# Optimization experiments

Hardware: AMD Instinct MI355X
Metric: run time of the kernel (lower is better)

Reference implementation:

```python
import jax, jax.numpy as jnp
import numpy as np

B, A, L, M, E = 4096, 64, 16, 4, 10
K = (4, 16, 32)
Q = (2, 4, 6)
P = (32, 128, 256)


def setup_inputs() -> dict:
    key = jax.random.key(0)
    ks = iter(jax.random.split(key, 32))
    inp = {}
    inp['x'] = jax.random.normal(next(ks), (B, A, L, M), dtype=jnp.float32)
    inp['y'] = jax.random.uniform(next(ks), (B, E), dtype=jnp.float32)
    inp['w1'] = jax.random.normal(next(ks), (E, K[0], Q[0], A), dtype=jnp.float32) / (K[0] * Q[0])
    inp['w2'] = jax.random.normal(next(ks), (E, K[1], Q[1], A), dtype=jnp.float32) / (K[1] * Q[1])
    inp['w3'] = jax.random.normal(next(ks), (E, K[2], Q[2], A), dtype=jnp.float32) / (K[2] * Q[2])
    inp['coeff1'] = jax.random.normal(next(ks), (P[0],), dtype=jnp.float32)
    inp['coeff2'] = jax.random.normal(next(ks), (P[1],), dtype=jnp.float32)
    inp['coeff3'] = jax.random.normal(next(ks), (P[2],), dtype=jnp.float32)
    ri = lambda n, hi: jax.random.randint(next(ks), (n,), 0, hi, dtype=jnp.int32)
    inp['i1'] = ri(P[0], L); inp['l1'] = ri(P[0], M)
    inp['k1'] = ri(P[0], K[0]); inp['q1'] = ri(P[0], Q[0])
    inp['i2'] = ri(P[1], L); inp['j2'] = ri(P[1], L)
    inp['l2'] = ri(P[1], M); inp['m2'] = ri(P[1], M)
    inp['k2'] = ri(P[1], K[1]); inp['q2'] = ri(P[1], Q[1])
    inp['i3'] = ri(P[2], L); inp['j3'] = ri(P[2], L); inp['f3'] = ri(P[2], L)
    inp['l3'] = ri(P[2], M); inp['m3'] = ri(P[2], M); inp['g3'] = ri(P[2], M)
    inp['k3'] = ri(P[2], K[2]); inp['q3'] = ri(P[2], Q[2])
    return inp


def _forward(x, y, w1, w2, w3, coeff1, coeff2, coeff3,
             i1, l1, k1, q1,
             i2, j2, l2, m2, k2, q2,
             i3, j3, f3, l3, m3, g3, k3, q3):
    # element-mixed weights: [B, K, Q, A]
    wy1 = jnp.einsum('ekqa,be->bkqa', w1, y)
    wy2 = jnp.einsum('ekqa,be->bkqa', w2, y)
    wy3 = jnp.einsum('ekqa,be->bkqa', w3, y)
    # sparse path contraction (equivalent to dense 'ik,lq,ekqa,bail,be->ba' etc.)
    g1 = jnp.transpose(wy1[:, k1, q1, :], (0, 2, 1))          # [B, A, P1]
    t1 = jnp.einsum('bap,p->ba', x[:, :, i1, l1] * g1, coeff1)
    g2 = jnp.transpose(wy2[:, k2, q2, :], (0, 2, 1))          # [B, A, P2]
    t2 = jnp.einsum('bap,p->ba', x[:, :, i2, l2] * x[:, :, j2, m2] * g2, coeff2)
    g3_ = jnp.transpose(wy3[:, k3, q3, :], (0, 2, 1))         # [B, A, P3]
    t3 = jnp.einsum('bap,p->ba',
                    x[:, :, i3, l3] * x[:, :, j3, m3] * x[:, :, f3, g3] * g3_,
                    coeff3)
    return t1 + t2 + t3  # [B, A] (scalar irrep_out -> flattened view)


def reference(x, y, w1, w2, w3, coeff1, coeff2, coeff3,
              i1, l1, k1, q1,
              i2, j2, l2, m2, k2, q2,
              i3, j3, f3, l3, m3, g3, k3, q3):
    return _forward(x, y, w1, w2, w3, coeff1, coeff2, coeff3,
                    i1, l1, k1, q1,
                    i2, j2, l2, m2, k2, q2,
                    i3, j3, f3, l3, m3, g3, k3, q3)
```

## Files before the change

### kernel.cpp

```cpp
#include <hip/hip_runtime.h>
#include <hip/hip_bf16.h>

typedef _Float16 f16x8 __attribute__((ext_vector_type(8)));
typedef _Float16 f16x4 __attribute__((ext_vector_type(4)));
typedef float    f32x4 __attribute__((ext_vector_type(4)));

constexpr int BB  = 4096;
constexpr int AA  = 64;
constexpr int ED  = 10;
constexpr int P1N = 32, P2N = 128, P3N = 256;
constexpr int PT  = 416;
constexpr int NKS = 13;
constexpr int BCH = 64;
constexpr int NCH = 4;

__global__ void build_idx_kernel(
    const int* __restrict__ i1, const int* __restrict__ l1,
    const int* __restrict__ i2, const int* __restrict__ j2,
    const int* __restrict__ l2, const int* __restrict__ m2,
    const int* __restrict__ i3, const int* __restrict__ j3,
    const int* __restrict__ f3, const int* __restrict__ l3,
    const int* __restrict__ m3, const int* __restrict__ g3,
    unsigned* __restrict__ idxs) {
  const int p = threadIdx.x;
  if (p >= PT) return;
  unsigned sa, sb = 64, sc = 64;
  if (p < P1N) {
    sa = i1[p] * 4 + l1[p];
  } else if (p < P1N + P2N) {
    int pp = p - P1N;
    sa = i2[pp] * 4 + l2[pp];
    sb = j2[pp] * 4 + m2[pp];
  } else {
    int pp = p - P1N - P2N;
    sa = i3[pp] * 4 + l3[pp];
    sb = j3[pp] * 4 + m3[pp];
    sc = f3[pp] * 4 + g3[pp];
  }
  idxs[p] = (sa * 8) | ((sb * 8) << 10) | ((sc * 8) << 20);
}

__global__ void build_cwb_kernel(
    const float* __restrict__ w1, const float* __restrict__ w2, const float* __restrict__ w3,
    const float* __restrict__ c1, const float* __restrict__ c2, const float* __restrict__ c3,
    const int* __restrict__ k1, const int* __restrict__ q1,
    const int* __restrict__ k2, const int* __restrict__ q2,
    const int* __restrict__ k3, const int* __restrict__ q3,
    _Float16* __restrict__ cwb) {
  const int a  = blockIdx.x & 63;
  const int ks = blockIdx.x >> 6;
  const int l  = threadIdx.x;
  const int grp = l >> 4, e = l & 15;
  _Float16* dst = cwb + (((size_t)a * NKS + ks) * 64 + l) * 8;
  #pragma unroll
  for (int j = 0; j < 8; ++j) {
    const int p = ks * 32 + grp * 8 + j;
    float v = 0.f;
    if (e < ED) {
      const float* w; float coeff; int k, q, K, Q;
      if (p < P1N)            { w = w1; coeff = c1[p]; k = k1[p]; q = q1[p]; K = 4;  Q = 2; }
      else if (p < P1N + P2N) { int pp = p - P1N;       w = w2; coeff = c2[pp]; k = k2[pp]; q = q2[pp]; K = 16; Q = 4; }
      else                    { int pp = p - P1N - P2N; w = w3; coeff = c3[pp]; k = k3[pp]; q = q3[pp]; K = 32; Q = 6; }
      v = coeff * w[(((size_t)e * K + k) * Q + q) * AA + a];
    }
    dst[j] = (_Float16)v;
  }
}

template <int NF, int KS>
__device__ __forceinline__ void kstep(
    const char* __restrict__ rowb, const uint4* __restrict__ ip,
    const f16x8* __restrict__ cw0, const f16x8* __restrict__ cw1,
    const f16x8* __restrict__ cw2, const f16x8* __restrict__ cw3,
    f32x4& ac0, f32x4& ac1, f32x4& ac2, f32x4& ac3) {
  const uint4 iA = ip[KS * 8 + 0];
  const uint4 iB = ip[KS * 8 + 1];
  const f16x8 b0 = cw0[KS * 64];
  const f16x8 b1 = cw1[KS * 64];
  const f16x8 b2 = cw2[KS * 64];
  const f16x8 b3 = cw3[KS * 64];
  const unsigned pks[8] = {iA.x, iA.y, iA.z, iA.w, iB.x, iB.y, iB.z, iB.w};
  f16x8 af0, af1, af2, af3;
  #pragma unroll
  for (int jh = 0; jh < 2; ++jh) {
    f16x4 g0[4], g1[4], g2[4];
    #pragma unroll
    for (int j = 0; j < 4; ++j) {
      const unsigned pk = pks[jh * 4 + j];
      g0[j] = *(const f16x4*)(rowb + (pk & 1023u));
      if (NF >= 2) g1[j] = *(const f16x4*)(rowb + ((pk >> 10) & 1023u));
      if (NF >= 3) g2[j] = *(const f16x4*)(rowb + (pk >> 20));
    }
    #pragma unroll
    for (int j = 0; j < 4; ++j) {
      f16x4 v = g0[j];
      if (NF >= 2) v = v * g1[j];
      if (NF >= 3) v = v * g2[j];
      const int jj = jh * 4 + j;
      af0[jj] = v[0]; af1[jj] = v[1]; af2[jj] = v[2]; af3[jj] = v[3];
    }
  }
  ac0 = __builtin_amdgcn_mfma_f32_16x16x32_f16(af0, b0, ac0, 0, 0, 0);
  ac1 = __builtin_amdgcn_mfma_f32_16x16x32_f16(af1, b1, ac1, 0, 0, 0);
  ac2 = __builtin_amdgcn_mfma_f32_16x16x32_f16(af2, b2, ac2, 0, 0, 0);
  ac3 = __builtin_amdgcn_mfma_f32_16x16x32_f16(af3, b3, ac3, 0, 0, 0);
}

__global__ __launch_bounds__(256, 4)
void contract_kernel(const float* __restrict__ x, const float* __restrict__ y,
                     const unsigned* __restrict__ idxs,
                     const f16x8* __restrict__ cwb,
                     float* __restrict__ out) {
  __shared__ f16x4 xls[BCH][65];
  __shared__ float yls[BCH][17];

  const int t  = threadIdx.x;
  const int a0 = (blockIdx.x & 15) * NCH;
  const int b0 = (blockIdx.x >> 4) * BCH;
  const int wv = t >> 6, l = t & 63, grp = l >> 4, er = l & 15;
  const int r0 = wv * 16;

  #pragma unroll
  for (int i = 0; i < 4; ++i) {
    const int row = r0 + i * 4 + (l >> 4);
    const int s   = (l & 15) * 4;
    const float* xb = x + (size_t)(b0 + row) * 4096 + a0 * 64 + s;
    const float4 L0 = *(const float4*)(xb);
    const float4 L1 = *(const float4*)(xb + 64);
    const float4 L2 = *(const float4*)(xb + 128);
    const float4 L3 = *(const float4*)(xb + 192);
    f16x4 v0, v1, v2, v3;
    v0[0] = (_Float16)L0.x; v0[1] = (_Float16)L1.x; v0[2] = (_Float16)L2.x; v0[3] = (_Float16)L3.x;
    v1[0] = (_Float16)L0.y; v1[1] = (_Float16)L1.y; v1[2] = (_Float16)L2.y; v1[3] = (_Float16)L3.y;
    v2[0] = (_Float16)L0.z; v2[1] = (_Float16)L1.z; v2[2] = (_Float16)L2.z; v2[3] = (_Float16)L3.z;
    v3[0] = (_Float16)L0.w; v3[1] = (_Float16)L1.w; v3[2] = (_Float16)L2.w; v3[3] = (_Float16)L3.w;
    xls[row][s + 0] = v0;
    xls[row][s + 1] = v1;
    xls[row][s + 2] = v2;
    xls[row][s + 3] = v3;
  }
  if (l < 16) {
    f16x4 one;
    one[0] = one[1] = one[2] = one[3] = (_Float16)1.0f;
    xls[r0 + l][64] = one;
    const float* yb = y + (size_t)(b0 + r0 + l) * ED;
    #pragma unroll
    for (int e = 0; e < ED; ++e) yls[r0 + l][e] = yb[e];
    #pragma unroll
    for (int e = ED; e < 16; ++e) yls[r0 + l][e] = 0.f;
  }

  const char* __restrict__ rowb = (const char*)&xls[r0 + er][0];
  const f16x8* __restrict__ cw0 = cwb + ((size_t)(a0 + 0) * NKS) * 64 + l;
  const f16x8* __restrict__ cw1 = cwb + ((size_t)(a0 + 1) * NKS) * 64 + l;
  const f16x8* __restrict__ cw2 = cwb + ((size_t)(a0 + 2) * NKS) * 64 + l;
  const f16x8* __restrict__ cw3 = cwb + ((size_t)(a0 + 3) * NKS) * 64 + l;
  const uint4*  __restrict__ ip  = (const uint4*)idxs + grp * 2;

  f32x4 ac0 = {0.f, 0.f, 0.f, 0.f};
  f32x4 ac1 = {0.f, 0.f, 0.f, 0.f};
  f32x4 ac2 = {0.f, 0.f, 0.f, 0.f};
  f32x4 ac3 = {0.f, 0.f, 0.f, 0.f};

  #define STEP(NF, KS) \
    kstep<NF, KS>(rowb, ip, cw0, cw1, cw2, cw3, ac0, ac1, ac2, ac3)
  STEP(1, 0);
  STEP(2, 1); STEP(2, 2); STEP(2, 3); STEP(2, 4);
  STEP(3, 5); STEP(3, 6); STEP(3, 7); STEP(3, 8);
  STEP(3, 9); STEP(3, 10); STEP(3, 11); STEP(3, 12);
  #undef STEP

  #pragma unroll
  for (int c = 0; c < NCH; ++c) {
    const f32x4 acc = c == 0 ? ac0 : c == 1 ? ac1 : c == 2 ? ac2 : ac3;
    float s0 = acc[0] * yls[r0 + grp * 4 + 0][er];
    float s1 = acc[1] * yls[r0 + grp * 4 + 1][er];
    float s2 = acc[2] * yls[r0 + grp * 4 + 2][er];
    float s3 = acc[3] * yls[r0 + grp * 4 + 3][er];
    #pragma unroll
    for (int m = 1; m < 16; m <<= 1) {
      s0 += __shfl_xor(s0, m);
      s1 += __shfl_xor(s1, m);
      s2 += __shfl_xor(s2, m);
      s3 += __shfl_xor(s3, m);
    }
    if (er < 4) {
      const float sv = er == 0 ? s0 : er == 1 ? s1 : er == 2 ? s2 : s3;
      out[(size_t)(b0 + r0 + grp * 4 + er) * AA + (a0 + c)] = sv;
    }
  }
}

extern "C" void kernel_launch(void* const* d_in, const int* in_sizes, int n_in,
                              void* d_out, int out_size, void* d_ws, size_t ws_size,
                              hipStream_t stream) {
  const float* x  = (const float*)d_in[0];
  const float* y  = (const float*)d_in[1];
  const float* w1 = (const float*)d_in[2];
  const float* w2 = (const float*)d_in[3];
  const float* w3 = (const float*)d_in[4];
  const float* c1 = (const float*)d_in[5];
  const float* c2 = (const float*)d_in[6];
  const float* c3 = (const float*)d_in[7];
  const int* i1 = (const int*)d_in[8];
  const int* l1 = (const int*)d_in[9];
  const int* k1 = (const int*)d_in[10];
  const int* q1 = (const int*)d_in[11];
  const int* i2 = (const int*)d_in[12];
  const int* j2 = (const int*)d_in[13];
  const int* l2 = (const int*)d_in[14];
  const int* m2 = (const int*)d_in[15];
  const int* k2 = (const int*)d_in[16];
  const int* q2 = (const int*)d_in[17];
  const int* i3 = (const int*)d_in[18];
  const int* j3 = (const int*)d_in[19];
  const int* f3 = (const int*)d_in[20];
  const int* l3 = (const int*)d_in[21];
  const int* m3 = (const int*)d_in[22];
  const int* g3 = (const int*)d_in[23];
  const int* k3 = (const int*)d_in[24];
  const int* q3 = (const int*)d_in[25];

  unsigned*  idxs = (unsigned*)d_ws;
  _Float16*  cwb  = (_Float16*)((char*)d_ws + 4096);

  build_idx_kernel<<<1, 448, 0, stream>>>(i1, l1, i2, j2, l2, m2,
                                          i3, j3, f3, l3, m3, g3, idxs);
  build_cwb_kernel<<<AA * NKS, 64, 0, stream>>>(w1, w2, w3, c1, c2, c3,
                                                k1, q1, k2, q2, k3, q3, cwb);
  contract_kernel<<<(AA / NCH) * (BB / BCH), 256, 0, stream>>>(
      x, y, idxs, (const f16x8*)cwb, (float*)d_out);
}
```

Baseline: 38.82 us.

## Split the K loop across wave pairs and halve the batch chunk per block

Each block now covers 32 batch rows instead of 64, which doubles the block count. The 13 MFMA k-steps are split between two waves per 16-row tile: one wave runs steps 0–6 and the other runs steps 7–12. Partial accumulators are combined through LDS scratch that reuses the x tile buffer, and the occupancy hint rises to 6 blocks. The aim is more parallelism and latency hiding, at the cost of extra barriers and an LDS reduction in every block.

```diff
diff --git a/kernel.cpp b/kernel.cpp
--- a/kernel.cpp
+++ b/kernel.cpp
@@ -11,7 +11,8 @@
 constexpr int P1N = 32, P2N = 128, P3N = 256;
 constexpr int PT  = 416;
 constexpr int NKS = 13;
-constexpr int BCH = 64;
+constexpr int KSPL = 7;
+constexpr int BCH = 32;
 constexpr int NCH = 4;
 
 __global__ void build_idx_kernel(
@@ -106,7 +107,7 @@
   ac3 = __builtin_amdgcn_mfma_f32_16x16x32_f16(af3, b3, ac3, 0, 0, 0);
 }
 
-__global__ __launch_bounds__(256, 4)
+__global__ __launch_bounds__(256, 6)
 void contract_kernel(const float* __restrict__ x, const float* __restrict__ y,
                      const unsigned* __restrict__ idxs,
                      const f16x8* __restrict__ cwb,
@@ -118,11 +119,10 @@
   const int a0 = (blockIdx.x & 15) * NCH;
   const int b0 = (blockIdx.x >> 4) * BCH;
   const int wv = t >> 6, l = t & 63, grp = l >> 4, er = l & 15;
-  const int r0 = wv * 16;
 
   #pragma unroll
-  for (int i = 0; i < 4; ++i) {
-    const int row = r0 + i * 4 + (l >> 4);
+  for (int i = 0; i < 2; ++i) {
+    const int row = wv * 8 + i * 4 + (l >> 4);
     const int s   = (l & 15) * 4;
     const float* xb = x + (size_t)(b0 + row) * 4096 + a0 * 64 + s;
     const float4 L0 = *(const float4*)(xb);
@@ -139,17 +139,22 @@
     xls[row][s + 2] = v2;
     xls[row][s + 3] = v3;
   }
-  if (l < 16) {
+  if (l < 8) {
+    const int row = wv * 8 + l;
     f16x4 one;
     one[0] = one[1] = one[2] = one[3] = (_Float16)1.0f;
-    xls[r0 + l][64] = one;
-    const float* yb = y + (size_t)(b0 + r0 + l) * ED;
-    #pragma unroll
-    for (int e = 0; e < ED; ++e) yls[r0 + l][e] = yb[e];
-    #pragma unroll
-    for (int e = ED; e < 16; ++e) yls[r0 + l][e] = 0.f;
-  }
-
+    xls[row][64] = one;
+    const float* yb = y + (size_t)(b0 + row) * ED;
+    #pragma unroll
+    for (int e = 0; e < ED; ++e) yls[row][e] = yb[e];
+    #pragma unroll
+    for (int e = ED; e < 16; ++e) yls[row][e] = 0.f;
+  }
+  __syncthreads();
+
+  const int mt = wv & 1;
+  const int kh = wv >> 1;
+  const int r0 = mt * 16;
   const char* __restrict__ rowb = (const char*)&xls[r0 + er][0];
   const f16x8* __restrict__ cw0 = cwb + ((size_t)(a0 + 0) * NKS) * 64 + l;
   const f16x8* __restrict__ cw1 = cwb + ((size_t)(a0 + 1) * NKS) * 64 + l;
@@ -164,29 +169,55 @@
 
   #define STEP(NF, KS) \
     kstep<NF, KS>(rowb, ip, cw0, cw1, cw2, cw3, ac0, ac1, ac2, ac3)
-  STEP(1, 0);
-  STEP(2, 1); STEP(2, 2); STEP(2, 3); STEP(2, 4);
-  STEP(3, 5); STEP(3, 6); STEP(3, 7); STEP(3, 8);
-  STEP(3, 9); STEP(3, 10); STEP(3, 11); STEP(3, 12);
+  if (kh == 0) {
+    STEP(1, 0);
+    STEP(2, 1); STEP(2, 2); STEP(2, 3); STEP(2, 4);
+    STEP(3, 5); STEP(3, 6);
+  } else {
+    STEP(3, 7); STEP(3, 8); STEP(3, 9);
+    STEP(3, 10); STEP(3, 11); STEP(3, 12);
+  }
   #undef STEP
 
-  #pragma unroll
-  for (int c = 0; c < NCH; ++c) {
-    const f32x4 acc = c == 0 ? ac0 : c == 1 ? ac1 : c == 2 ? ac2 : ac3;
-    float s0 = acc[0] * yls[r0 + grp * 4 + 0][er];
-    float s1 = acc[1] * yls[r0 + grp * 4 + 1][er];
-    float s2 = acc[2] * yls[r0 + grp * 4 + 2][er];
-    float s3 = acc[3] * yls[r0 + grp * 4 + 3][er];
-    #pragma unroll
-    for (int m = 1; m < 16; m <<= 1) {
-      s0 += __shfl_xor(s0, m);
-      s1 += __shfl_xor(s1, m);
-      s2 += __shfl_xor(s2, m);
-      s3 += __shfl_xor(s3, m);
-    }
-    if (er < 4) {
-      const float sv = er == 0 ? s0 : er == 1 ? s1 : er == 2 ? s2 : s3;
-      out[(size_t)(b0 + r0 + grp * 4 + er) * AA + (a0 + c)] = sv;
+  __syncthreads();
+  float* scr = (float*)&xls[0][0];
+  const int sbase = (mt * 64 + l) * 17;
+  if (kh == 1) {
+    #pragma unroll
+    for (int v = 0; v < 4; ++v) {
+      scr[sbase + v + 0]  = ac0[v];
+      scr[sbase + v + 4]  = ac1[v];
+      scr[sbase + v + 8]  = ac2[v];
+      scr[sbase + v + 12] = ac3[v];
+    }
+  }
+  __syncthreads();
+  if (kh == 0) {
+    #pragma unroll
+    for (int v = 0; v < 4; ++v) {
+      ac0[v] += scr[sbase + v + 0];
+      ac1[v] += scr[sbase + v + 4];
+      ac2[v] += scr[sbase + v + 8];
+      ac3[v] += scr[sbase + v + 12];
+    }
+    #pragma unroll
+    for (int c = 0; c < NCH; ++c) {
+      const f32x4 acc = c == 0 ? ac0 : c == 1 ? ac1 : c == 2 ? ac2 : ac3;
+      float s0 = acc[0] * yls[r0 + grp * 4 + 0][er];
+      float s1 = acc[1] * yls[r0 + grp * 4 + 1][er];
+      float s2 = acc[2] * yls[r0 + grp * 4 + 2][er];
+      float s3 = acc[3] * yls[r0 + grp * 4 + 3][er];
+      #pragma unroll
+      for (int m = 1; m < 16; m <<= 1) {
+        s0 += __shfl_xor(s0, m);
+        s1 += __shfl_xor(s1, m);
+        s2 += __shfl_xor(s2, m);
+        s3 += __shfl_xor(s3, m);
+      }
+      if (er < 4) {
+        const float sv = er == 0 ? s0 : er == 1 ? s1 : er == 2 ? s2 : s3;
+        out[(size_t)(b0 + r0 + grp * 4 + er) * AA + (a0 + c)] = sv;
+      }
     }
   }
 }
```

Result: slower. 43.05 us (+10.9%).
